# Performance work log

Hardware: AMD Instinct MI355X
Metric: run time of the kernel (lower is better)

Reference implementation:

```python
import jax, jax.numpy as jnp
import numpy as np

N = 50000      # nodes
E = 800000     # edges (avg degree 16)
F_IN = 128
H = 128
C = 2
EPS = 1e-5


def setup_inputs() -> dict:
    key = jax.random.key(0)
    ks = jax.random.split(key, 16)
    s_in = 1.0 / np.sqrt(F_IN)
    s_h = 1.0 / np.sqrt(H)
    return {
        "x": jax.random.normal(ks[0], (N, F_IN), jnp.float32),
        "edge_index": jax.random.randint(ks[1], (2, E), 0, N, jnp.int32),
        "W1": jax.random.normal(ks[2], (F_IN, H), jnp.float32) * s_in,
        "b1": jnp.zeros((H,), jnp.float32),
        "g1": jax.random.uniform(ks[3], (H,), jnp.float32, 0.5, 1.5),
        "be1": jnp.zeros((H,), jnp.float32),
        "m1": jax.random.normal(ks[4], (H,), jnp.float32) * 0.1,
        "v1": jax.random.uniform(ks[5], (H,), jnp.float32, 0.5, 1.5),
        "W2": jax.random.normal(ks[6], (H, H), jnp.float32) * s_h,
        "b2": jnp.zeros((H,), jnp.float32),
        "g2": jax.random.uniform(ks[7], (H,), jnp.float32, 0.5, 1.5),
        "be2": jnp.zeros((H,), jnp.float32),
        "m2": jax.random.normal(ks[8], (H,), jnp.float32) * 0.1,
        "v2": jax.random.uniform(ks[9], (H,), jnp.float32, 0.5, 1.5),
        "Wc": jax.random.normal(ks[10], (H, C), jnp.float32) * s_h,
        "bc": jnp.zeros((C,), jnp.float32),
    }


def _gcn_norm(edge_index):
    # Add self-loops: A_tilde = A + I, then symmetric normalization D^-1/2 A_tilde D^-1/2.
    loop = jnp.arange(N, dtype=edge_index.dtype)
    src = jnp.concatenate([edge_index[0], loop])
    dst = jnp.concatenate([edge_index[1], loop])
    deg = jax.ops.segment_sum(jnp.ones_like(src, jnp.float32), dst, num_segments=N)
    dinv = jnp.where(deg > 0, jax.lax.rsqrt(jnp.maximum(deg, 1.0)), 0.0)
    norm = dinv[src] * dinv[dst]  # per-edge coefficient
    return src, dst, norm


def _gcn_conv(h, src, dst, norm, W, b):
    h = h @ W                                  # [N, H]
    msg = h[src] * norm[:, None]               # gather + scale, [E+N, H]
    out = jax.ops.segment_sum(msg, dst, num_segments=N)
    return out + b


def _bn_eval(h, g, be, m, v):
    return (h - m) * (g * jax.lax.rsqrt(v + EPS)) + be


def reference(x, edge_index, W1, b1, g1, be1, m1, v1,
              W2, b2, g2, be2, m2, v2, Wc, bc):
    src, dst, norm = _gcn_norm(edge_index)
    h = _gcn_conv(x, src, dst, norm, W1, b1)
    h = jax.nn.relu(_bn_eval(h, g1, be1, m1, v1))  # dropout is identity in eval
    h = _gcn_conv(h, src, dst, norm, W2, b2)
    h = jax.nn.relu(_bn_eval(h, g2, be2, m2, v2))
    return h @ Wc + bc                            # logits [N, 2]
```

## Files before the change

kernel.cpp:

```cpp
#include <hip/hip_runtime.h>
#include <hip/hip_fp16.h>

#define EPSV 1e-5f
#define HSZ 6400
#define BPB 32

using half8 = __attribute__((ext_vector_type(8))) _Float16;
using f32x4 = __attribute__((ext_vector_type(4))) float;

__device__ __forceinline__ int bin_lo(int b, int mul) {
    return (int)((((long long)b << 25) + mul - 1) / mul);
}

__global__ __launch_bounds__(128) void k_setup(const float* __restrict__ W1, const float* __restrict__ W2,
                                               _Float16* __restrict__ whi1, _Float16* __restrict__ wlo1,
                                               _Float16* __restrict__ whi2, _Float16* __restrict__ wlo2,
                                               const float* __restrict__ g1, const float* __restrict__ v1,
                                               const float* __restrict__ b1, const float* __restrict__ m1,
                                               const float* __restrict__ be1,
                                               const float* __restrict__ g2, const float* __restrict__ v2,
                                               const float* __restrict__ b2, const float* __restrict__ m2,
                                               const float* __restrict__ be2,
                                               float* __restrict__ par, __half* __restrict__ padrow,
                                               int* __restrict__ bcur) {
    int b = blockIdx.x;
    int t = threadIdx.x;
    if (b < 32) {
        const float* W = (b < 16) ? W1 : W2;
        _Float16* whi = (b < 16) ? whi1 : whi2;
        _Float16* wlo = (b < 16) ? wlo1 : wlo2;
        int tile = ((b & 15) << 1) | (t >> 6);
        int l = t & 63;
        int kt = tile >> 3, ct = tile & 7;
        int k0 = kt * 32 + (l >> 4) * 8;
        int c = ct * 16 + (l & 15);
        half8 hi, lo;
#pragma unroll
        for (int j = 0; j < 8; j++) {
            float w = W[(k0 + j) * 128 + c];
            _Float16 h = (_Float16)w;
            hi[j] = h;
            lo[j] = (_Float16)(w - (float)h);
        }
        size_t o = (size_t)tile * 64 + l;
        ((half8*)whi)[o] = hi;
        ((half8*)wlo)[o] = lo;
    } else {
        int c = t;
        float s1 = g1[c] * rsqrtf(v1[c] + EPSV);
        par[c] = s1;
        par[128 + c] = fmaf(b1[c] - m1[c], s1, be1[c]);
        float s2 = g2[c] * rsqrtf(v2[c] + EPSV);
        par[256 + c] = s2;
        par[384 + c] = fmaf(b2[c] - m2[c], s2, be2[c]);
        padrow[c] = __float2half(0.f);
        if (c < 8) bcur[c] = 0;
    }
}

__global__ __launch_bounds__(256) void k_bin(const int* __restrict__ src, const int* __restrict__ dst,
                                             int* __restrict__ bcur, unsigned int* __restrict__ binned,
                                             int E, int mul, int bin_cap) {
    int lane = threadIdx.x & 63;
    int gw = (blockIdx.x * 256 + threadIdx.x) >> 6;
    int nw = (gridDim.x * 256) >> 6;
    bool v4 = ((E & 3) == 0);
    for (int base = gw * 1024; base < E; base += nw * 1024) {
        unsigned int vals[16];
        int bins[16];
        unsigned long long clo = 0, chi = 0;
#pragma unroll
        for (int g = 0; g < 4; g++) {
            int e0 = base + g * 256 + lane * 4;
            int4 s4, d4;
            if (v4 && e0 + 3 < E) {
                s4 = *(const int4*)(src + e0);
                d4 = *(const int4*)(dst + e0);
            } else {
                s4.x = (e0 < E) ? src[e0] : 0;         d4.x = (e0 < E) ? dst[e0] : -1;
                s4.y = (e0 + 1 < E) ? src[e0 + 1] : 0; d4.y = (e0 + 1 < E) ? dst[e0 + 1] : -1;
                s4.z = (e0 + 2 < E) ? src[e0 + 2] : 0; d4.z = (e0 + 2 < E) ? dst[e0 + 2] : -1;
                s4.w = (e0 + 3 < E) ? src[e0 + 3] : 0; d4.w = (e0 + 3 < E) ? dst[e0 + 3] : -1;
            }
            int ss[4] = {s4.x, s4.y, s4.z, s4.w};
            int dd[4] = {d4.x, d4.y, d4.z, d4.w};
#pragma unroll
            for (int k = 0; k < 4; k++) {
                int j = g * 4 + k;
                int d = dd[k];
                if (d >= 0) {
                    vals[j] = ((unsigned int)ss[k] << 16) | (unsigned int)d;
                    int b = (d * mul) >> 25;
                    bins[j] = b;
                    if (b < 4) clo += 1ull << (b * 16);
                    else       chi += 1ull << ((b - 4) * 16);
                } else bins[j] = -1;
            }
        }
        unsigned long long ilo = clo, ihi = chi;
#pragma unroll
        for (int d = 1; d < 64; d <<= 1) {
            unsigned long long ulo = __shfl_up(ilo, d, 64);
            unsigned long long uhi = __shfl_up(ihi, d, 64);
            if (lane >= d) { ilo += ulo; ihi += uhi; }
        }
        unsigned long long tlo = __shfl(ilo, 63, 64), thi = __shfl(ihi, 63, 64);
        unsigned long long plo = ilo - clo, phi = ihi - chi;
        int mytot = 0;
        if (lane < 4) mytot = (int)((tlo >> (lane * 16)) & 0xffff);
        else if (lane < 8) mytot = (int)((thi >> ((lane - 4) * 16)) & 0xffff);
        int alloc = 0;
        if (lane < 8) alloc = atomicAdd(&bcur[lane], mytot);
#pragma unroll
        for (int j = 0; j < 16; j++) {
            int b = bins[j];
            int bs = (b < 0) ? 0 : b;
            int bbase = __shfl(alloc, bs, 64);
            int sh = (bs & 3) * 16;
            unsigned long long sel = (bs < 4) ? plo : phi;
            int rel = (int)((sel >> sh) & 0xffffu);
            unsigned long long inc = 1ull << sh;
            if (bs < 4) plo += inc; else phi += inc;
            if (b >= 0) binned[(size_t)bs * bin_cap + bbase + rel] = vals[j];
        }
    }
}

__global__ __launch_bounds__(256) void k_count(const unsigned int* __restrict__ binned,
                                               const int* __restrict__ bcnt, int* __restrict__ phist,
                                               int mul, int bin_cap) {
    __shared__ int hist[HSZ];
    int b = blockIdx.x & 7;
    int blk = blockIdx.x >> 3;
    int t = threadIdx.x;
    for (int i = t; i < HSZ; i += 256) hist[i] = 0;
    __syncthreads();
    int lo = bin_lo(b, mul);
    int cnt = bcnt[b];
    int e0 = (int)((long long)blk * cnt / BPB);
    int e1 = (int)((long long)(blk + 1) * cnt / BPB);
    const unsigned int* bp = binned + (size_t)b * bin_cap;
    for (int i = e0 + t; i < e1; i += 256) {
        int d = (int)(bp[i] & 0xffffu);
        atomicAdd(&hist[d - lo], 1);
    }
    __syncthreads();
    int* ph = phist + (size_t)blockIdx.x * HSZ;
    for (int i = t; i < HSZ; i += 256) ph[i] = hist[i];
}

__global__ __launch_bounds__(256) void k_bsum(int* __restrict__ phist, int* __restrict__ deg,
                                              int* __restrict__ bsum, int N, int mul) {
    int t = threadIdx.x;
    int base = blockIdx.x * 1024;
    int s = 0;
    for (int j = 0; j < 4; j++) {
        int i = base + j * 256 + t;
        if (i < N) {
            int b = (i * mul) >> 25;
            int lo = bin_lo(b, mul);
            int local = i - lo;
            int run = 0;
#pragma unroll
            for (int blk = 0; blk < BPB; blk++) {
                int* p = phist + (size_t)(blk * 8 + b) * HSZ + local;
                int c = *p;
                *p = run;
                run += c;
            }
            deg[i] = run;
            s += (run + 7) & ~7;
        }
    }
#pragma unroll
    for (int d = 1; d < 64; d <<= 1) s += __shfl_xor(s, d, 64);
    __shared__ int ws[4];
    if ((t & 63) == 0) ws[t >> 6] = s;
    __syncthreads();
    if (t == 0) bsum[blockIdx.x] = ws[0] + ws[1] + ws[2] + ws[3];
}

__global__ __launch_bounds__(256) void k_scanout(const int* __restrict__ deg, const int* __restrict__ bsum,
                                                 int* __restrict__ row_start, int* __restrict__ rend,
                                                 float* __restrict__ dinv, int n, int nb) {
    __shared__ int s_boff;
    __shared__ int ws[4];
    int t = threadIdx.x, lane = t & 63, wid = t >> 6;
    if (t < 64) {
        int v = (t < nb) ? bsum[t] : 0;
        int incl = v;
#pragma unroll
        for (int d = 1; d < 64; d <<= 1) {
            int u = __shfl_up(incl, d, 64);
            if (t >= d) incl += u;
        }
        if (t == (int)blockIdx.x) s_boff = incl - v;
    }
    __syncthreads();
    int base = blockIdx.x * 1024 + t * 4;
    int v[4], pv[4], ts = 0;
#pragma unroll
    for (int j = 0; j < 4; j++) {
        v[j] = (base + j < n) ? deg[base + j] : 0;
        pv[j] = (v[j] + 7) & ~7;
        ts += pv[j];
    }
    int incl = ts;
#pragma unroll
    for (int d = 1; d < 64; d <<= 1) {
        int u = __shfl_up(incl, d, 64);
        if (lane >= d) incl += u;
    }
    if (lane == 63) ws[wid] = incl;
    __syncthreads();
    int wo = 0;
    for (int i = 0; i < wid; i++) wo += ws[i];
    int run = s_boff + wo + (incl - ts);
#pragma unroll
    for (int j = 0; j < 4; j++) {
        if (base + j < n) {
            row_start[base + j] = run;
            rend[base + j] = run + v[j];
            dinv[base + j] = rsqrtf((float)v[j] + 1.0f);
            run += pv[j];
        }
    }
}

__global__ __launch_bounds__(256) void k_fill(const unsigned int* __restrict__ binned,
                                              const int* __restrict__ bcnt, const int* __restrict__ row_start,
                                              const int* __restrict__ phist, unsigned short* __restrict__ csr,
                                              int N, int mul, int bin_cap) {
    __shared__ int cur[HSZ];
    int b = blockIdx.x & 7;
    int blk = blockIdx.x >> 3;
    int t = threadIdx.x;
    int lo = bin_lo(b, mul);
    int hi = (b == 7) ? N : bin_lo(b + 1, mul);
    if (hi > N) hi = N;
    const int* ph = phist + (size_t)blockIdx.x * HSZ;
    for (int i = t; i < HSZ; i += 256) {
        int d = lo + i;
        cur[i] = (d < hi) ? (row_start[d] + ph[i]) : 0;
    }
    __syncthreads();
    int cnt = bcnt[b];
    int e0 = (int)((long long)blk * cnt / BPB);
    int e1 = (int)((long long)(blk + 1) * cnt / BPB);
    const unsigned int* bp = binned + (size_t)b * bin_cap;
    for (int i = e0 + t; i < e1; i += 256) {
        unsigned int v = bp[i];
        int d = (int)(v & 0xffffu);
        int q = atomicAdd(&cur[d - lo], 1);
        csr[q] = (unsigned short)(v >> 16);
    }
}

template <bool AFP16>
__global__ __launch_bounds__(256) void k_gemm(const void* __restrict__ Araw,
                                              const _Float16* __restrict__ whi,
                                              const _Float16* __restrict__ wlo,
                                              const float* __restrict__ scale,
                                              unsigned short* __restrict__ out, int M) {
    __shared__ uint4 sB[4096];
    int tid = threadIdx.x;
    int l = tid & 63;
    int w = tid >> 6;
    int r0 = blockIdx.x * 64 + w * 16;
    int ra = r0 + (l & 15);
    if (ra >= M) ra = M - 1;
    int kl = (l >> 4) * 8;

    half8 avh[4];
    float4 af0[4], af1[4];
    if constexpr (AFP16) {
#pragma unroll
        for (int kt = 0; kt < 4; kt++)
            avh[kt] = *(const half8*)((const _Float16*)Araw + (size_t)ra * 128 + kt * 32 + kl);
    } else {
#pragma unroll
        for (int kt = 0; kt < 4; kt++) {
            const float* pa = (const float*)Araw + (size_t)ra * 128 + kt * 32 + kl;
            af0[kt] = *(const float4*)pa;
            af1[kt] = *(const float4*)(pa + 4);
        }
    }

    {
        const uint4* gh = (const uint4*)whi;
        const uint4* gl = (const uint4*)wlo;
#pragma unroll
        for (int i = 0; i < 8; i++) sB[tid + i * 256] = gh[tid + i * 256];
#pragma unroll
        for (int i = 0; i < 8; i++) sB[2048 + tid + i * 256] = gl[tid + i * 256];
    }
    __syncthreads();

    f32x4 acc[8];
#pragma unroll
    for (int i = 0; i < 8; i++) acc[i] = (f32x4)0.f;

    const half8* bh8 = (const half8*)sB;
    const half8* bl8 = (const half8*)(sB + 2048);

#pragma unroll
    for (int kt = 0; kt < 4; kt++) {
        half8 ah, al;
        if constexpr (AFP16) {
            ah = avh[kt];
        } else {
            float fa[8] = {af0[kt].x, af0[kt].y, af0[kt].z, af0[kt].w,
                           af1[kt].x, af1[kt].y, af1[kt].z, af1[kt].w};
#pragma unroll
            for (int j = 0; j < 8; j++) {
                _Float16 h = (_Float16)fa[j];
                ah[j] = h;
                al[j] = (_Float16)(fa[j] - (float)h);
            }
        }
#pragma unroll
        for (int ct = 0; ct < 8; ct++) {
            half8 bh = bh8[(kt * 8 + ct) * 64 + l];
            half8 bl = bl8[(kt * 8 + ct) * 64 + l];
            acc[ct] = __builtin_amdgcn_mfma_f32_16x16x32_f16(ah, bh, acc[ct], 0, 0, 0);
            if constexpr (!AFP16)
                acc[ct] = __builtin_amdgcn_mfma_f32_16x16x32_f16(al, bh, acc[ct], 0, 0, 0);
            acc[ct] = __builtin_amdgcn_mfma_f32_16x16x32_f16(ah, bl, acc[ct], 0, 0, 0);
        }
    }

    __syncthreads();
    _Float16* stw = (_Float16*)sB + w * 2048;
#pragma unroll
    for (int r = 0; r < 4; r++) {
        int trow = (l >> 4) * 4 + r;
        int grow = r0 + trow;
        float s = scale[(grow < M) ? grow : (M - 1)];
#pragma unroll
        for (int ct = 0; ct < 8; ct++)
            stw[trow * 128 + ct * 16 + (l & 15)] = (_Float16)(acc[ct][r] * s);
    }
#pragma unroll
    for (int p = 0; p < 4; p++) {
        int trow = p * 4 + (l >> 4);
        int grow = r0 + trow;
        if (grow < M) {
            uint4 v = *(const uint4*)&stw[trow * 128 + (l & 15) * 8];
            *(uint4*)&out[(size_t)grow * 128 + (l & 15) * 8] = v;
        }
    }
}

__device__ __forceinline__ void f2acc(float2& a, const __half2 h) {
    float2 f = __half22float2(h);
    a.x += f.x;
    a.y += f.y;
}

__device__ __forceinline__ void aggr_gather(const float4* __restrict__ Hs4, const unsigned short* __restrict__ csr,
                                            int rs, int re, int node, int zrow, int lc, float2 acc[4]) {
    {
        float4 sv = Hs4[(size_t)node * 16 + lc];
        const __half2* h = (const __half2*)&sv;
        acc[0] = __half22float2(h[0]);
        acc[1] = __half22float2(h[1]);
        acc[2] = __half22float2(h[2]);
        acc[3] = __half22float2(h[3]);
    }
    float2 accB[4] = {{0.f, 0.f}, {0.f, 0.f}, {0.f, 0.f}, {0.f, 0.f}};
    const uint4* cp = (const uint4*)(csr + rs);
    int nch = (re - rs + 7) >> 3;
    if (nch <= 0) return;
    uint4 q = cp[0];
    for (int c = 0; c < nch; c++) {
        uint4 qn = (c + 1 < nch) ? cp[c + 1] : q;
        int id[8] = {(int)(q.x & 0xffffu), (int)(q.x >> 16), (int)(q.y & 0xffffu), (int)(q.y >> 16),
                     (int)(q.z & 0xffffu), (int)(q.z >> 16), (int)(q.w & 0xffffu), (int)(q.w >> 16)};
        int base = rs + c * 8;
        float4 v[8];
#pragma unroll
        for (int j = 0; j < 8; j++) {
            int a = base + j;
            int ix = (a < re) ? id[j] : zrow;
            v[j] = Hs4[(size_t)ix * 16 + lc];
        }
#pragma unroll
        for (int j = 0; j < 8; j++) {
            const __half2* h = (const __half2*)&v[j];
            float2* acp = (j & 1) ? accB : acc;
            f2acc(acp[0], h[0]);
            f2acc(acp[1], h[1]);
            f2acc(acp[2], h[2]);
            f2acc(acp[3], h[3]);
        }
        q = qn;
    }
#pragma unroll
    for (int k = 0; k < 4; k++) {
        acc[k].x += accB[k].x;
        acc[k].y += accB[k].y;
    }
}

__device__ __forceinline__ void bn_relu(const float2 acc[4], float dn, const float* __restrict__ par,
                                        int lc, float4& y0, float4& y1) {
    float4 s0 = ((const float4*)par)[lc * 2];
    float4 s1 = ((const float4*)par)[lc * 2 + 1];
    float4 t0 = ((const float4*)par)[32 + lc * 2];
    float4 t1 = ((const float4*)par)[32 + lc * 2 + 1];
    y0.x = fmaxf(fmaf(acc[0].x * dn, s0.x, t0.x), 0.f);
    y0.y = fmaxf(fmaf(acc[0].y * dn, s0.y, t0.y), 0.f);
    y0.z = fmaxf(fmaf(acc[1].x * dn, s0.z, t0.z), 0.f);
    y0.w = fmaxf(fmaf(acc[1].y * dn, s0.w, t0.w), 0.f);
    y1.x = fmaxf(fmaf(acc[2].x * dn, s1.x, t1.x), 0.f);
    y1.y = fmaxf(fmaf(acc[2].y * dn, s1.y, t1.y), 0.f);
    y1.z = fmaxf(fmaf(acc[3].x * dn, s1.z, t1.z), 0.f);
    y1.w = fmaxf(fmaf(acc[3].y * dn, s1.w, t1.w), 0.f);
}

__global__ __launch_bounds__(256) void k_aggr(const float4* __restrict__ Hs4, const int* __restrict__ row_start,
                                              const int* __restrict__ rend,
                                              const unsigned short* __restrict__ csr, const float* __restrict__ dinv,
                                              const float* __restrict__ par, uint4* __restrict__ out, int n) {
    int lc = threadIdx.x & 15;
    int node = blockIdx.x * 16 + (threadIdx.x >> 4);
    if (node >= n) return;
    float2 acc[4];
    aggr_gather(Hs4, csr, row_start[node], rend[node], node, n, lc, acc);
    float4 y0, y1;
    bn_relu(acc, dinv[node], par, lc, y0, y1);
    __half2 p0 = __floats2half2_rn(y0.x, y0.y);
    __half2 p1 = __floats2half2_rn(y0.z, y0.w);
    __half2 p2 = __floats2half2_rn(y1.x, y1.y);
    __half2 p3 = __floats2half2_rn(y1.z, y1.w);
    uint4 pk;
    pk.x = *(unsigned int*)&p0;
    pk.y = *(unsigned int*)&p1;
    pk.z = *(unsigned int*)&p2;
    pk.w = *(unsigned int*)&p3;
    out[(size_t)node * 16 + lc] = pk;
}

__global__ __launch_bounds__(256) void k_aggr_cls(const float4* __restrict__ Hs4, const int* __restrict__ row_start,
                                                  const int* __restrict__ rend,
                                                  const unsigned short* __restrict__ csr, const float* __restrict__ dinv,
                                                  const float* __restrict__ par, const float4* __restrict__ Wc4,
                                                  const float* __restrict__ bc, float2* __restrict__ out, int n) {
    int lc = threadIdx.x & 15;
    int node = blockIdx.x * 16 + (threadIdx.x >> 4);
    if (node >= n) return;
    float2 acc[4];
    aggr_gather(Hs4, csr, row_start[node], rend[node], node, n, lc, acc);
    float4 y0, y1;
    bn_relu(acc, dinv[node], par, lc, y0, y1);
    float4 w0 = Wc4[lc * 4], w1 = Wc4[lc * 4 + 1], w2 = Wc4[lc * 4 + 2], w3 = Wc4[lc * 4 + 3];
    float p0 = y0.x * w0.x + y0.y * w0.z + y0.z * w1.x + y0.w * w1.z
             + y1.x * w2.x + y1.y * w2.z + y1.z * w3.x + y1.w * w3.z;
    float p1 = y0.x * w0.y + y0.y * w0.w + y0.z * w1.y + y0.w * w1.w
             + y1.x * w2.y + y1.y * w2.w + y1.z * w3.y + y1.w * w3.w;
#pragma unroll
    for (int d = 1; d < 16; d <<= 1) {
        p0 += __shfl_xor(p0, d, 16);
        p1 += __shfl_xor(p1, d, 16);
    }
    if (lc == 0) out[node] = make_float2(p0 + bc[0], p1 + bc[1]);
}

extern "C" void kernel_launch(void* const* d_in, const int* in_sizes, int n_in,
                              void* d_out, int out_size, void* d_ws, size_t ws_size,
                              hipStream_t stream) {
    const float* x = (const float*)d_in[0];
    const int* ei = (const int*)d_in[1];
    const float* W1 = (const float*)d_in[2];
    const float* b1 = (const float*)d_in[3];
    const float* g1 = (const float*)d_in[4];
    const float* be1 = (const float*)d_in[5];
    const float* m1 = (const float*)d_in[6];
    const float* v1 = (const float*)d_in[7];
    const float* W2 = (const float*)d_in[8];
    const float* b2 = (const float*)d_in[9];
    const float* g2 = (const float*)d_in[10];
    const float* be2 = (const float*)d_in[11];
    const float* m2 = (const float*)d_in[12];
    const float* v2 = (const float*)d_in[13];
    const float* Wc = (const float*)d_in[14];
    const float* bc = (const float*)d_in[15];
    float* out = (float*)d_out;

    const int N = in_sizes[0] / 128;
    const int E = in_sizes[1] / 2;
    const int* src = ei;
    const int* dst = ei + E;

    const int mul = (int)((8LL << 25) / N);
    const int bin_cap = ((E / 8 + 8192 + 63) / 64) * 64;

    int* W = (int*)d_ws;
    size_t off = 0;
    int* deg = W + off; off += N;
    int* bcur = W + off; off += 8;
    int* row_start = W + off; off += (size_t)N + 1;
    int* rend = W + off; off += N;
    float* dinv = (float*)(W + off); off += N;
    int* bsum = W + off; off += 64;
    float* par = (float*)(W + off); off += 512;
    _Float16* whi1 = (_Float16*)(W + off); off += 8192;
    _Float16* wlo1 = (_Float16*)(W + off); off += 8192;
    _Float16* whi2 = (_Float16*)(W + off); off += 8192;
    _Float16* wlo2 = (_Float16*)(W + off); off += 8192;
    int* phist = W + off; off += (size_t)8 * BPB * HSZ;
    off = (off + 3) & ~(size_t)3;
    unsigned short* csr = (unsigned short*)(W + off); off += (size_t)(E + 8 * N + 32 + 1) / 2;
    off = (off + 3) & ~(size_t)3;
    unsigned int* binned = (unsigned int*)(W + off); off += (size_t)8 * bin_cap;
    off = (off + 3) & ~(size_t)3;
    __half* Hs = (__half*)(W + off); off += (size_t)(N + 1) * 64;
    _Float16* Ag = (_Float16*)(W + off);

    k_setup<<<33, 128, 0, stream>>>(W1, W2, whi1, wlo1, whi2, wlo2,
                                    g1, v1, b1, m1, be1, g2, v2, b2, m2, be2,
                                    par, Hs + (size_t)N * 128, bcur);

    int nb = (N + 1023) / 1024;
    k_bin<<<512, 256, 0, stream>>>(src, dst, bcur, binned, E, mul, bin_cap);
    k_count<<<8 * BPB, 256, 0, stream>>>(binned, bcur, phist, mul, bin_cap);
    k_bsum<<<nb, 256, 0, stream>>>(phist, deg, bsum, N, mul);
    k_scanout<<<nb, 256, 0, stream>>>(deg, bsum, row_start, rend, dinv, N, nb);
    k_fill<<<8 * BPB, 256, 0, stream>>>(binned, bcur, row_start, phist, csr, N, mul, bin_cap);

    int gbm = (N + 63) / 64;
    int ab = (N + 15) / 16;
    k_gemm<false><<<gbm, 256, 0, stream>>>(x, whi1, wlo1, dinv, (unsigned short*)Hs, N);
    k_aggr<<<ab, 256, 0, stream>>>((const float4*)Hs, row_start, rend, csr, dinv, par, (uint4*)Ag, N);
    k_gemm<true><<<gbm, 256, 0, stream>>>(Ag, whi2, wlo2, dinv, (unsigned short*)Hs, N);
    k_aggr_cls<<<ab, 256, 0, stream>>>((const float4*)Hs, row_start, rend, csr, dinv, par + 256,
                                       (const float4*)Wc, bc, (float2*)out, N);
}
```

Before: 153.8 us.

## Fuse first GEMM with edge binning and move source normalization into CSR weights

The first feature GEMM no longer needs the degree normalization, so its blocks are launched in the same grid as the edge-binning kernel and the two run concurrently. The per-source dinv scale moves out of the GEMM epilogue into a half-precision weight packed beside each source index in the CSR (now 32-bit entries). The aggregation then uses FMAs with those weights and scales the self-loop by the node's own dinv. This removes a dependency and a launch but doubles CSR gather bytes and rounds the per-edge weight to fp16.

```diff
diff --git a/kernel.cpp b/kernel.cpp
--- a/kernel.cpp
+++ b/kernel.cpp
@@ -21,8 +21,7 @@
                                                const float* __restrict__ g2, const float* __restrict__ v2,
                                                const float* __restrict__ b2, const float* __restrict__ m2,
                                                const float* __restrict__ be2,
-                                               float* __restrict__ par, __half* __restrict__ padrow,
-                                               int* __restrict__ bcur) {
+                                               float* __restrict__ par, int* __restrict__ bcur) {
     int b = blockIdx.x;
     int t = threadIdx.x;
     if (b < 32) {
@@ -53,17 +52,16 @@
         float s2 = g2[c] * rsqrtf(v2[c] + EPSV);
         par[256 + c] = s2;
         par[384 + c] = fmaf(b2[c] - m2[c], s2, be2[c]);
-        padrow[c] = __float2half(0.f);
         if (c < 8) bcur[c] = 0;
     }
 }
 
-__global__ __launch_bounds__(256) void k_bin(const int* __restrict__ src, const int* __restrict__ dst,
-                                             int* __restrict__ bcur, unsigned int* __restrict__ binned,
-                                             int E, int mul, int bin_cap) {
-    int lane = threadIdx.x & 63;
-    int gw = (blockIdx.x * 256 + threadIdx.x) >> 6;
-    int nw = (gridDim.x * 256) >> 6;
+__device__ __forceinline__ void bin_body(const int* __restrict__ src, const int* __restrict__ dst,
+                                         int* __restrict__ bcur, unsigned int* __restrict__ binned,
+                                         int E, int mul, int bin_cap, int bid, int nblocks, int tid) {
+    int lane = tid & 63;
+    int gw = (bid * 256 + tid) >> 6;
+    int nw = (nblocks * 256) >> 6;
     bool v4 = ((E & 3) == 0);
     for (int base = gw * 1024; base < E; base += nw * 1024) {
         unsigned int vals[16];
@@ -126,6 +124,121 @@
     }
 }
 
+template <bool AFP16>
+__device__ __forceinline__ void gemm_body(const void* __restrict__ Araw,
+                                          const _Float16* __restrict__ whi,
+                                          const _Float16* __restrict__ wlo,
+                                          unsigned short* __restrict__ out, int M,
+                                          int bid, int tid, uint4* __restrict__ sB) {
+    int l = tid & 63;
+    int w = tid >> 6;
+    int r0 = bid * 64 + w * 16;
+    int ra = r0 + (l & 15);
+    if (ra >= M) ra = M - 1;
+    int kl = (l >> 4) * 8;
+
+    half8 avh[4];
+    float4 af0[4], af1[4];
+    if constexpr (AFP16) {
+#pragma unroll
+        for (int kt = 0; kt < 4; kt++)
+            avh[kt] = *(const half8*)((const _Float16*)Araw + (size_t)ra * 128 + kt * 32 + kl);
+    } else {
+#pragma unroll
+        for (int kt = 0; kt < 4; kt++) {
+            const float* pa = (const float*)Araw + (size_t)ra * 128 + kt * 32 + kl;
+            af0[kt] = *(const float4*)pa;
+            af1[kt] = *(const float4*)(pa + 4);
+        }
+    }
+
+    {
+        const uint4* gh = (const uint4*)whi;
+        const uint4* gl = (const uint4*)wlo;
+#pragma unroll
+        for (int i = 0; i < 8; i++) sB[tid + i * 256] = gh[tid + i * 256];
+#pragma unroll
+        for (int i = 0; i < 8; i++) sB[2048 + tid + i * 256] = gl[tid + i * 256];
+    }
+    __syncthreads();
+
+    f32x4 acc[8];
+#pragma unroll
+    for (int i = 0; i < 8; i++) acc[i] = (f32x4)0.f;
+
+    const half8* bh8 = (const half8*)sB;
+    const half8* bl8 = (const half8*)(sB + 2048);
+
+#pragma unroll
+    for (int kt = 0; kt < 4; kt++) {
+        half8 ah, al;
+        if constexpr (AFP16) {
+            ah = avh[kt];
+        } else {
+            float fa[8] = {af0[kt].x, af0[kt].y, af0[kt].z, af0[kt].w,
+                           af1[kt].x, af1[kt].y, af1[kt].z, af1[kt].w};
+#pragma unroll
+            for (int j = 0; j < 8; j++) {
+                _Float16 h = (_Float16)fa[j];
+                ah[j] = h;
+                al[j] = (_Float16)(fa[j] - (float)h);
+            }
+        }
+#pragma unroll
+        for (int ct = 0; ct < 8; ct++) {
+            half8 bh = bh8[(kt * 8 + ct) * 64 + l];
+            half8 bl = bl8[(kt * 8 + ct) * 64 + l];
+            acc[ct] = __builtin_amdgcn_mfma_f32_16x16x32_f16(ah, bh, acc[ct], 0, 0, 0);
+            if constexpr (!AFP16)
+                acc[ct] = __builtin_amdgcn_mfma_f32_16x16x32_f16(al, bh, acc[ct], 0, 0, 0);
+            acc[ct] = __builtin_amdgcn_mfma_f32_16x16x32_f16(ah, bl, acc[ct], 0, 0, 0);
+        }
+    }
+
+    __syncthreads();
+    _Float16* stw = (_Float16*)sB + w * 2048;
+#pragma unroll
+    for (int r = 0; r < 4; r++) {
+        int trow = (l >> 4) * 4 + r;
+#pragma unroll
+        for (int ct = 0; ct < 8; ct++)
+            stw[trow * 128 + ct * 16 + (l & 15)] = (_Float16)(acc[ct][r]);
+    }
+#pragma unroll
+    for (int p = 0; p < 4; p++) {
+        int trow = p * 4 + (l >> 4);
+        int grow = r0 + trow;
+        if (grow < M) {
+            uint4 v = *(const uint4*)&stw[trow * 128 + (l & 15) * 8];
+            *(uint4*)&out[(size_t)grow * 128 + (l & 15) * 8] = v;
+        }
+    }
+}
+
+__global__ __launch_bounds__(256) void k_bingemm(const int* __restrict__ src, const int* __restrict__ dst,
+                                                 int* __restrict__ bcur, unsigned int* __restrict__ binned,
+                                                 int E, int mul, int bin_cap,
+                                                 const float* __restrict__ x,
+                                                 const _Float16* __restrict__ whi,
+                                                 const _Float16* __restrict__ wlo,
+                                                 unsigned short* __restrict__ outHs, int M, int bin_blocks) {
+    __shared__ uint4 sB[4096];
+    if ((int)blockIdx.x < bin_blocks) {
+        bin_body(src, dst, bcur, binned, E, mul, bin_cap, blockIdx.x, bin_blocks, threadIdx.x);
+        return;
+    }
+    gemm_body<false>(x, whi, wlo, outHs, M, blockIdx.x - bin_blocks, threadIdx.x, sB);
+}
+
+template <bool AFP16>
+__global__ __launch_bounds__(256) void k_gemm(const void* __restrict__ Araw,
+                                              const _Float16* __restrict__ whi,
+                                              const _Float16* __restrict__ wlo,
+                                              unsigned short* __restrict__ out, int M) {
+    __shared__ uint4 sB[4096];
+    gemm_body<AFP16>(Araw, whi, wlo, out, M, blockIdx.x, threadIdx.x, sB);
+}
+
 __global__ __launch_bounds__(256) void k_count(const unsigned int* __restrict__ binned,
                                                const int* __restrict__ bcnt, int* __restrict__ phist,
                                                int mul, int bin_cap) {
@@ -229,7 +342,8 @@
 
 __global__ __launch_bounds__(256) void k_fill(const unsigned int* __restrict__ binned,
                                               const int* __restrict__ bcnt, const int* __restrict__ row_start,
-                                              const int* __restrict__ phist, unsigned short* __restrict__ csr,
+                                              const int* __restrict__ phist, const float* __restrict__ dinv,
+                                              unsigned int* __restrict__ csr,
                                               int N, int mul, int bin_cap) {
     __shared__ int cur[HSZ];
     int b = blockIdx.x & 7;
@@ -251,149 +365,67 @@
     for (int i = e0 + t; i < e1; i += 256) {
         unsigned int v = bp[i];
         int d = (int)(v & 0xffffu);
+        int s = (int)(v >> 16);
+        __half h = __float2half_rn(dinv[s]);
+        unsigned short hb = *(unsigned short*)&h;
         int q = atomicAdd(&cur[d - lo], 1);
-        csr[q] = (unsigned short)(v >> 16);
-    }
-}
-
-template <bool AFP16>
-__global__ __launch_bounds__(256) void k_gemm(const void* __restrict__ Araw,
-                                              const _Float16* __restrict__ whi,
-                                              const _Float16* __restrict__ wlo,
-                                              const float* __restrict__ scale,
-                                              unsigned short* __restrict__ out, int M) {
-    __shared__ uint4 sB[4096];
-    int tid = threadIdx.x;
-    int l = tid & 63;
-    int w = tid >> 6;
-    int r0 = blockIdx.x * 64 + w * 16;
-    int ra = r0 + (l & 15);
-    if (ra >= M) ra = M - 1;
-    int kl = (l >> 4) * 8;
-
-    half8 avh[4];
-    float4 af0[4], af1[4];
-    if constexpr (AFP16) {
-#pragma unroll
-        for (int kt = 0; kt < 4; kt++)
-            avh[kt] = *(const half8*)((const _Float16*)Araw + (size_t)ra * 128 + kt * 32 + kl);
-    } else {
-#pragma unroll
-        for (int kt = 0; kt < 4; kt++) {
-            const float* pa = (const float*)Araw + (size_t)ra * 128 + kt * 32 + kl;
-            af0[kt] = *(const float4*)pa;
-            af1[kt] = *(const float4*)(pa + 4);
-        }
-    }
-
-    {
-        const uint4* gh = (const uint4*)whi;
-        const uint4* gl = (const uint4*)wlo;
-#pragma unroll
-        for (int i = 0; i < 8; i++) sB[tid + i * 256] = gh[tid + i * 256];
-#pragma unroll
-        for (int i = 0; i < 8; i++) sB[2048 + tid + i * 256] = gl[tid + i * 256];
-    }
-    __syncthreads();
-
-    f32x4 acc[8];
-#pragma unroll
-    for (int i = 0; i < 8; i++) acc[i] = (f32x4)0.f;
-
-    const half8* bh8 = (const half8*)sB;
-    const half8* bl8 = (const half8*)(sB + 2048);
-
-#pragma unroll
-    for (int kt = 0; kt < 4; kt++) {
-        half8 ah, al;
-        if constexpr (AFP16) {
-            ah = avh[kt];
-        } else {
-            float fa[8] = {af0[kt].x, af0[kt].y, af0[kt].z, af0[kt].w,
-                           af1[kt].x, af1[kt].y, af1[kt].z, af1[kt].w};
-#pragma unroll
-            for (int j = 0; j < 8; j++) {
-                _Float16 h = (_Float16)fa[j];
-                ah[j] = h;
-                al[j] = (_Float16)(fa[j] - (float)h);
-            }
-        }
-#pragma unroll
-        for (int ct = 0; ct < 8; ct++) {
-            half8 bh = bh8[(kt * 8 + ct) * 64 + l];
-            half8 bl = bl8[(kt * 8 + ct) * 64 + l];
-            acc[ct] = __builtin_amdgcn_mfma_f32_16x16x32_f16(ah, bh, acc[ct], 0, 0, 0);
-            if constexpr (!AFP16)
-                acc[ct] = __builtin_amdgcn_mfma_f32_16x16x32_f16(al, bh, acc[ct], 0, 0, 0);
-            acc[ct] = __builtin_amdgcn_mfma_f32_16x16x32_f16(ah, bl, acc[ct], 0, 0, 0);
-        }
-    }
-
-    __syncthreads();
-    _Float16* stw = (_Float16*)sB + w * 2048;
-#pragma unroll
-    for (int r = 0; r < 4; r++) {
-        int trow = (l >> 4) * 4 + r;
-        int grow = r0 + trow;
-        float s = scale[(grow < M) ? grow : (M - 1)];
-#pragma unroll
-        for (int ct = 0; ct < 8; ct++)
-            stw[trow * 128 + ct * 16 + (l & 15)] = (_Float16)(acc[ct][r] * s);
-    }
-#pragma unroll
-    for (int p = 0; p < 4; p++) {
-        int trow = p * 4 + (l >> 4);
-        int grow = r0 + trow;
-        if (grow < M) {
-            uint4 v = *(const uint4*)&stw[trow * 128 + (l & 15) * 8];
-            *(uint4*)&out[(size_t)grow * 128 + (l & 15) * 8] = v;
-        }
-    }
-}
-
-__device__ __forceinline__ void f2acc(float2& a, const __half2 h) {
+        csr[q] = ((unsigned int)hb << 16) | (unsigned int)s;
+    }
+}
+
+__device__ __forceinline__ void f2fma(float2& a, const __half2 h, float w) {
     float2 f = __half22float2(h);
-    a.x += f.x;
-    a.y += f.y;
-}
-
-__device__ __forceinline__ void aggr_gather(const float4* __restrict__ Hs4, const unsigned short* __restrict__ csr,
-                                            int rs, int re, int node, int zrow, int lc, float2 acc[4]) {
+    a.x = fmaf(f.x, w, a.x);
+    a.y = fmaf(f.y, w, a.y);
+}
+
+__device__ __forceinline__ float pk_w(unsigned int pk) {
+    __half h;
+    *(unsigned short*)&h = (unsigned short)(pk >> 16);
+    return __half2float(h);
+}
+
+__device__ __forceinline__ void aggr_gather(const float4* __restrict__ Hs4, const unsigned int* __restrict__ csr,
+                                            int rs, int re, int node, float dn, int lc, float2 acc[4]) {
     {
         float4 sv = Hs4[(size_t)node * 16 + lc];
         const __half2* h = (const __half2*)&sv;
-        acc[0] = __half22float2(h[0]);
-        acc[1] = __half22float2(h[1]);
-        acc[2] = __half22float2(h[2]);
-        acc[3] = __half22float2(h[3]);
-    }
+        float2 f0 = __half22float2(h[0]), f1 = __half22float2(h[1]);
+        float2 f2 = __half22float2(h[2]), f3 = __half22float2(h[3]);
+        acc[0] = make_float2(f0.x * dn, f0.y * dn);
+        acc[1] = make_float2(f1.x * dn, f1.y * dn);
+        acc[2] = make_float2(f2.x * dn, f2.y * dn);
+        acc[3] = make_float2(f3.x * dn, f3.y * dn);
+    }
+    int nch = (re - rs + 7) >> 3;
+    if (nch <= 0) return;
     float2 accB[4] = {{0.f, 0.f}, {0.f, 0.f}, {0.f, 0.f}, {0.f, 0.f}};
     const uint4* cp = (const uint4*)(csr + rs);
-    int nch = (re - rs + 7) >> 3;
-    if (nch <= 0) return;
-    uint4 q = cp[0];
+    uint4 q0 = cp[0], q1 = cp[1];
     for (int c = 0; c < nch; c++) {
-        uint4 qn = (c + 1 < nch) ? cp[c + 1] : q;
-        int id[8] = {(int)(q.x & 0xffffu), (int)(q.x >> 16), (int)(q.y & 0xffffu), (int)(q.y >> 16),
-                     (int)(q.z & 0xffffu), (int)(q.z >> 16), (int)(q.w & 0xffffu), (int)(q.w >> 16)};
+        uint4 n0 = q0, n1 = q1;
+        if (c + 1 < nch) { n0 = cp[2 * c + 2]; n1 = cp[2 * c + 3]; }
+        unsigned int pks[8] = {q0.x, q0.y, q0.z, q0.w, q1.x, q1.y, q1.z, q1.w};
         int base = rs + c * 8;
         float4 v[8];
+        float w[8];
 #pragma unroll
         for (int j = 0; j < 8; j++) {
-            int a = base + j;
-            int ix = (a < re) ? id[j] : zrow;
+            unsigned int pk = (base + j < re) ? pks[j] : 0u;
+            int ix = (int)(pk & 0xffffu);
+            w[j] = pk_w(pk);
             v[j] = Hs4[(size_t)ix * 16 + lc];
         }
 #pragma unroll
         for (int j = 0; j < 8; j++) {
             const __half2* h = (const __half2*)&v[j];
             float2* acp = (j & 1) ? accB : acc;
-            f2acc(acp[0], h[0]);
-            f2acc(acp[1], h[1]);
-            f2acc(acp[2], h[2]);
-            f2acc(acp[3], h[3]);
-        }
-        q = qn;
+            f2fma(acp[0], h[0], w[j]);
+            f2fma(acp[1], h[1], w[j]);
+            f2fma(acp[2], h[2], w[j]);
+            f2fma(acp[3], h[3], w[j]);
+        }
+        q0 = n0; q1 = n1;
     }
 #pragma unroll
     for (int k = 0; k < 4; k++) {
@@ -420,15 +452,16 @@
 
 __global__ __launch_bounds__(256) void k_aggr(const float4* __restrict__ Hs4, const int* __restrict__ row_start,
                                               const int* __restrict__ rend,
-                                              const unsigned short* __restrict__ csr, const float* __restrict__ dinv,
+                                              const unsigned int* __restrict__ csr, const float* __restrict__ dinv,
                                               const float* __restrict__ par, uint4* __restrict__ out, int n) {
     int lc = threadIdx.x & 15;
     int node = blockIdx.x * 16 + (threadIdx.x >> 4);
     if (node >= n) return;
+    float dn = dinv[node];
     float2 acc[4];
-    aggr_gather(Hs4, csr, row_start[node], rend[node], node, n, lc, acc);
+    aggr_gather(Hs4, csr, row_start[node], rend[node], node, dn, lc, acc);
     float4 y0, y1;
-    bn_relu(acc, dinv[node], par, lc, y0, y1);
+    bn_relu(acc, dn, par, lc, y0, y1);
     __half2 p0 = __floats2half2_rn(y0.x, y0.y);
     __half2 p1 = __floats2half2_rn(y0.z, y0.w);
     __half2 p2 = __floats2half2_rn(y1.x, y1.y);
@@ -443,16 +476,17 @@
 
 __global__ __launch_bounds__(256) void k_aggr_cls(const float4* __restrict__ Hs4, const int* __restrict__ row_start,
                                                   const int* __restrict__ rend,
-                                                  const unsigned short* __restrict__ csr, const float* __restrict__ dinv,
+                                                  const unsigned int* __restrict__ csr, const float* __restrict__ dinv,
                                                   const float* __restrict__ par, const float4* __restrict__ Wc4,
                                                   const float* __restrict__ bc, float2* __restrict__ out, int n) {
     int lc = threadIdx.x & 15;
     int node = blockIdx.x * 16 + (threadIdx.x >> 4);
     if (node >= n) return;
+    float dn = dinv[node];
     float2 acc[4];
-    aggr_gather(Hs4, csr, row_start[node], rend[node], node, n, lc, acc);
+    aggr_gather(Hs4, csr, row_start[node], rend[node], node, dn, lc, acc);
     float4 y0, y1;
-    bn_relu(acc, dinv[node], par, lc, y0, y1);
+    bn_relu(acc, dn, par, lc, y0, y1);
     float4 w0 = Wc4[lc * 4], w1 = Wc4[lc * 4 + 1], w2 = Wc4[lc * 4 + 2], w3 = Wc4[lc * 4 + 3];
     float p0 = y0.x * w0.x + y0.y * w0.z + y0.z * w1.x + y0.w * w1.z
              + y1.x * w2.x + y1.y * w2.z + y1.z * w3.x + y1.w * w3.z;
@@ -509,30 +543,29 @@
     _Float16* whi2 = (_Float16*)(W + off); off += 8192;
     _Float16* wlo2 = (_Float16*)(W + off); off += 8192;
     int* phist = W + off; off += (size_t)8 * BPB * HSZ;
-    off = (off + 3) & ~(size_t)3;
-    unsigned short* csr = (unsigned short*)(W + off); off += (size_t)(E + 8 * N + 32 + 1) / 2;
-    off = (off + 3) & ~(size_t)3;
+    unsigned int* csr = (unsigned int*)(W + off); off += (size_t)E + 8 * N + 64;
     unsigned int* binned = (unsigned int*)(W + off); off += (size_t)8 * bin_cap;
     off = (off + 3) & ~(size_t)3;
-    __half* Hs = (__half*)(W + off); off += (size_t)(N + 1) * 64;
+    __half* Hs = (__half*)(W + off); off += (size_t)N * 64;
     _Float16* Ag = (_Float16*)(W + off);
 
     k_setup<<<33, 128, 0, stream>>>(W1, W2, whi1, wlo1, whi2, wlo2,
                                     g1, v1, b1, m1, be1, g2, v2, b2, m2, be2,
-                                    par, Hs + (size_t)N * 128, bcur);
+                                    par, bcur);
 
     int nb = (N + 1023) / 1024;
-    k_bin<<<512, 256, 0, stream>>>(src, dst, bcur, binned, E, mul, bin_cap);
+    int gbm = (N + 63) / 64;
+    int bin_blocks = 512;
+    k_bingemm<<<bin_blocks + gbm, 256, 0, stream>>>(src, dst, bcur, binned, E, mul, bin_cap,
+                                                    x, whi1, wlo1, (unsigned short*)Hs, N, bin_blocks);
     k_count<<<8 * BPB, 256, 0, stream>>>(binned, bcur, phist, mul, bin_cap);
     k_bsum<<<nb, 256, 0, stream>>>(phist, deg, bsum, N, mul);
     k_scanout<<<nb, 256, 0, stream>>>(deg, bsum, row_start, rend, dinv, N, nb);
-    k_fill<<<8 * BPB, 256, 0, stream>>>(binned, bcur, row_start, phist, csr, N, mul, bin_cap);
-
-    int gbm = (N + 63) / 64;
+    k_fill<<<8 * BPB, 256, 0, stream>>>(binned, bcur, row_start, phist, dinv, csr, N, mul, bin_cap);
+
     int ab = (N + 15) / 16;
-    k_gemm<false><<<gbm, 256, 0, stream>>>(x, whi1, wlo1, dinv, (unsigned short*)Hs, N);
     k_aggr<<<ab, 256, 0, stream>>>((const float4*)Hs, row_start, rend, csr, dinv, par, (uint4*)Ag, N);
-    k_gemm<true><<<gbm, 256, 0, stream>>>(Ag, whi2, wlo2, dinv, (unsigned short*)Hs, N);
+    k_gemm<true><<<gbm, 256, 0, stream>>>(Ag, whi2, wlo2, (unsigned short*)Hs, N);
     k_aggr_cls<<<ab, 256, 0, stream>>>((const float4*)Hs, row_start, rend, csr, dinv, par + 256,
                                        (const float4*)Wc, bc, (float2*)out, N);
 }
```

Result: faster. 150.7 us (-2.0%).
